# Kernel optimization log

Hardware: AMD Instinct MI355X
Metric: run time of the kernel (lower is better)

The kernel has to match this reference:

```python
import jax, jax.numpy as jnp
import numpy as np

SMOOTH = 1e-05


def setup_inputs() -> dict:
    key = jax.random.key(0)
    k1, k2, k3 = jax.random.split(key, 3)
    B, C, D, H, W = 2, 24, 96, 96, 96
    logit0 = jax.random.uniform(k1, (B, C, D, H, W), dtype=jnp.float32)
    target = jax.random.randint(k2, (B, 1, D, H, W), 0, C, dtype=jnp.int32)
    class_for_batch = jax.random.randint(k3, (12,), 0, C, dtype=jnp.int32)
    return {"logit0": logit0, "target": target, "class_for_batch": class_for_batch}


def reference(logit0, target, class_for_batch):
    B, C = logit0.shape[0], logit0.shape[1]
    # present[ch] = True iff ch in class_for_batch; channel 0 is never merged away
    present = jnp.zeros((C,), dtype=bool).at[class_for_batch].set(True).at[0].set(True)
    mask = present.astype(logit0.dtype)  # [C]
    # merge absent channels into channel 0, zero them out (fused masked-merge)
    absent_sum = jnp.einsum('bcdhw,c->bdhw', logit0, 1.0 - mask)
    logit = logit0 * mask[None, :, None, None, None]
    logit = logit.at[:, 0].add(absent_sum)
    # clamp, log, one-hot gather at target label
    logpt = jnp.log(jnp.clip(logit, SMOOTH, 1.0))  # [B,C,D,H,W]
    tgt = target[:, 0]  # [B,D,H,W]
    gathered = jnp.take_along_axis(logpt, tgt[:, None], axis=1)[:, 0]  # [B,D,H,W]
    ce = gathered + SMOOTH
    alpha = mask[tgt]  # 1 for present (and class 0), 0 for absent classes
    loss = (-alpha * ce).mean()
    return loss
```

## Files before the change

### kernel.cpp

```cpp
#include <hip/hip_runtime.h>

static constexpr int   kS = 96 * 96 * 96;
static constexpr int   kC = 24;
static constexpr int   kB = 2;
static constexpr int   kN = kB * kS;
static constexpr float kSmooth = 1e-5f;
static constexpr int   kThreads = 256;
static constexpr int   kBlocks  = (kN / 4) / kThreads;

__global__ __launch_bounds__(kThreads) void mce_kernel(
    const float* __restrict__ logit0,
    const int*   __restrict__ target,
    const int*   __restrict__ cfb,
    float*       __restrict__ ws)
{
    unsigned present = 1u;
#pragma unroll
    for (int i = 0; i < 12; ++i) present |= (1u << cfb[i]);

    const int g    = blockIdx.x * kThreads + threadIdx.x;
    const int base = g * 4;

    const int4 t4 = reinterpret_cast<const int4*>(target)[g];
    const int t[4] = { t4.x, t4.y, t4.z, t4.w };

    const int b  = (base >= kS) ? 1 : 0;
    const int s0 = base - b * kS;
    const float4* __restrict__ plane4 =
        reinterpret_cast<const float4*>(logit0 + (size_t)b * kC * kS + s0);

    float4 x[kC];
#pragma unroll
    for (int c = 0; c < kC; ++c)
        x[c] = plane4[(size_t)c * (kS / 4)];

    float4 asum = make_float4(0.f, 0.f, 0.f, 0.f);
    float4 vsel = make_float4(0.f, 0.f, 0.f, 0.f);
#pragma unroll
    for (int c = 0; c < kC; ++c) {
        const float af = ((present >> c) & 1u) ? 0.0f : 1.0f;
        asum.x = fmaf(af, x[c].x, asum.x);
        asum.y = fmaf(af, x[c].y, asum.y);
        asum.z = fmaf(af, x[c].z, asum.z);
        asum.w = fmaf(af, x[c].w, asum.w);
        vsel.x = (t[0] == c) ? x[c].x : vsel.x;
        vsel.y = (t[1] == c) ? x[c].y : vsel.y;
        vsel.z = (t[2] == c) ? x[c].z : vsel.z;
        vsel.w = (t[3] == c) ? x[c].w : vsel.w;
    }

    float acc = 0.0f;
    {
        const float vs[4] = { vsel.x, vsel.y, vsel.z, vsel.w };
        const float as[4] = { asum.x, asum.y, asum.z, asum.w };
#pragma unroll
        for (int j = 0; j < 4; ++j) {
            const int tj = t[j];
            float val = vs[j] + ((tj == 0) ? as[j] : 0.0f);
            val = fminf(fmaxf(val, kSmooth), 1.0f);
            const float ce = __logf(val) + kSmooth;
            acc += (((present >> tj) & 1u) ? ce : 0.0f);
        }
    }

#pragma unroll
    for (int off = 32; off > 0; off >>= 1)
        acc += __shfl_down(acc, off, 64);

    __shared__ float wave_sums[4];
    const int lane = threadIdx.x & 63;
    const int wid  = threadIdx.x >> 6;
    if (lane == 0) wave_sums[wid] = acc;
    __syncthreads();

    if (threadIdx.x == 0) {
        ws[blockIdx.x] = wave_sums[0] + wave_sums[1] + wave_sums[2] + wave_sums[3];
    }
}

__global__ __launch_bounds__(kThreads) void reduce_kernel(
    const float* __restrict__ ws, float* __restrict__ out)
{
    float acc = 0.0f;
    for (int i = threadIdx.x; i < kBlocks; i += kThreads) acc += ws[i];

#pragma unroll
    for (int off = 32; off > 0; off >>= 1)
        acc += __shfl_down(acc, off, 64);

    __shared__ float wave_sums[4];
    const int lane = threadIdx.x & 63;
    const int wid  = threadIdx.x >> 6;
    if (lane == 0) wave_sums[wid] = acc;
    __syncthreads();

    if (threadIdx.x == 0) {
        float s = wave_sums[0] + wave_sums[1] + wave_sums[2] + wave_sums[3];
        out[0] = s * (-1.0f / (float)kN);
    }
}

extern "C" void kernel_launch(void* const* d_in, const int* in_sizes, int n_in,
                              void* d_out, int out_size, void* d_ws, size_t ws_size,
                              hipStream_t stream)
{
    const float* logit0 = (const float*)d_in[0];
    const int*   target = (const int*)d_in[1];
    const int*   cfb    = (const int*)d_in[2];
    float*       out    = (float*)d_out;
    float*       ws     = (float*)d_ws;

    mce_kernel<<<kBlocks, kThreads, 0, stream>>>(logit0, target, cfb, ws);
    reduce_kernel<<<1, kThreads, 0, stream>>>(ws, out);
}
```

Measured before the change: 240.9 us.

## Process four quads per thread with double-buffered channel loads

Each thread now handles four float4 spatial quads (16 positions) instead of one, cutting the block count by four. Channel loads move from all 24 up front to a one-channel-ahead double buffer across the four quads, which keeps register pressure moderate while keeping loads in flight. This reduces per-block overhead and partial-sum writes, but may lower the number of outstanding memory requests per thread compared with issuing all 24 loads at once.

```diff
diff --git a/kernel.cpp b/kernel.cpp
--- a/kernel.cpp
+++ b/kernel.cpp
@@ -6,7 +6,9 @@
 static constexpr int   kN = kB * kS;
 static constexpr float kSmooth = 1e-5f;
 static constexpr int   kThreads = 256;
-static constexpr int   kBlocks  = (kN / 4) / kThreads;
+static constexpr int   kQuads   = 4;
+static constexpr int   kPosPerBlock = kThreads * kQuads * 4;
+static constexpr int   kBlocks  = kN / kPosPerBlock;
 
 __global__ __launch_bounds__(kThreads) void mce_kernel(
     const float* __restrict__ logit0,
@@ -18,44 +20,66 @@
 #pragma unroll
     for (int i = 0; i < 12; ++i) present |= (1u << cfb[i]);
 
-    const int g    = blockIdx.x * kThreads + threadIdx.x;
-    const int base = g * 4;
-
-    const int4 t4 = reinterpret_cast<const int4*>(target)[g];
-    const int t[4] = { t4.x, t4.y, t4.z, t4.w };
-
+    const int tid  = threadIdx.x;
+    const int base = blockIdx.x * kPosPerBlock;
     const int b  = (base >= kS) ? 1 : 0;
     const int s0 = base - b * kS;
+
+    const int4* __restrict__ tgt4 =
+        reinterpret_cast<const int4*>(target + (size_t)b * kS + s0);
+    int t[kQuads][4];
+#pragma unroll
+    for (int q = 0; q < kQuads; ++q) {
+        const int4 v = tgt4[q * kThreads + tid];
+        t[q][0] = v.x; t[q][1] = v.y; t[q][2] = v.z; t[q][3] = v.w;
+    }
+
     const float4* __restrict__ plane4 =
         reinterpret_cast<const float4*>(logit0 + (size_t)b * kC * kS + s0);
 
-    float4 x[kC];
+    float4 asum[kQuads], vsel[kQuads];
 #pragma unroll
-    for (int c = 0; c < kC; ++c)
-        x[c] = plane4[(size_t)c * (kS / 4)];
+    for (int q = 0; q < kQuads; ++q) {
+        asum[q] = make_float4(0.f, 0.f, 0.f, 0.f);
+        vsel[q] = make_float4(0.f, 0.f, 0.f, 0.f);
+    }
 
-    float4 asum = make_float4(0.f, 0.f, 0.f, 0.f);
-    float4 vsel = make_float4(0.f, 0.f, 0.f, 0.f);
+    float4 xa[kQuads], xb[kQuads];
+#pragma unroll
+    for (int q = 0; q < kQuads; ++q)
+        xa[q] = plane4[q * kThreads + tid];
+
 #pragma unroll
     for (int c = 0; c < kC; ++c) {
+        if (c + 1 < kC) {
+#pragma unroll
+            for (int q = 0; q < kQuads; ++q)
+                xb[q] = plane4[(size_t)(c + 1) * (kS / 4) + q * kThreads + tid];
+        }
         const float af = ((present >> c) & 1u) ? 0.0f : 1.0f;
-        asum.x = fmaf(af, x[c].x, asum.x);
-        asum.y = fmaf(af, x[c].y, asum.y);
-        asum.z = fmaf(af, x[c].z, asum.z);
-        asum.w = fmaf(af, x[c].w, asum.w);
-        vsel.x = (t[0] == c) ? x[c].x : vsel.x;
-        vsel.y = (t[1] == c) ? x[c].y : vsel.y;
-        vsel.z = (t[2] == c) ? x[c].z : vsel.z;
-        vsel.w = (t[3] == c) ? x[c].w : vsel.w;
+#pragma unroll
+        for (int q = 0; q < kQuads; ++q) {
+            asum[q].x = fmaf(af, xa[q].x, asum[q].x);
+            asum[q].y = fmaf(af, xa[q].y, asum[q].y);
+            asum[q].z = fmaf(af, xa[q].z, asum[q].z);
+            asum[q].w = fmaf(af, xa[q].w, asum[q].w);
+            vsel[q].x = (t[q][0] == c) ? xa[q].x : vsel[q].x;
+            vsel[q].y = (t[q][1] == c) ? xa[q].y : vsel[q].y;
+            vsel[q].z = (t[q][2] == c) ? xa[q].z : vsel[q].z;
+            vsel[q].w = (t[q][3] == c) ? xa[q].w : vsel[q].w;
+        }
+#pragma unroll
+        for (int q = 0; q < kQuads; ++q) xa[q] = xb[q];
     }
 
     float acc = 0.0f;
-    {
-        const float vs[4] = { vsel.x, vsel.y, vsel.z, vsel.w };
-        const float as[4] = { asum.x, asum.y, asum.z, asum.w };
+#pragma unroll
+    for (int q = 0; q < kQuads; ++q) {
+        const float vs[4] = { vsel[q].x, vsel[q].y, vsel[q].z, vsel[q].w };
+        const float as[4] = { asum[q].x, asum[q].y, asum[q].z, asum[q].w };
 #pragma unroll
         for (int j = 0; j < 4; ++j) {
-            const int tj = t[j];
+            const int tj = t[q][j];
             float val = vs[j] + ((tj == 0) ? as[j] : 0.0f);
             val = fminf(fmaxf(val, kSmooth), 1.0f);
             const float ce = __logf(val) + kSmooth;
```

Result: no change. 238.9 us (-0.8%).
